# Performance work log

Hardware: AMD Instinct MI355X
Metric: run time of the kernel (lower is better)

## Reference

```python
import jax, jax.numpy as jnp
import numpy as np

H = 16          # num_attention_heads
D = 64          # attention_head_size
BUCKET = 128    # bucket_size
MAX_BUCKETS = 32
TEMP = 0.75
SINKHORN_ITERS = 5
NOISE_KEY = 42  # fixed key for gumbel routing noise (deterministic reference)


def _sinkhorn_route(pl, W, key):
    # pl: [b,h,buckets,d] bucket summaries, W: [h,d,buckets]
    R = jnp.einsum('bhid,hdf->bhif', pl, W)  # [b,h,buckets,buckets]
    u = jax.random.uniform(key, R.shape, R.dtype)
    gumbel = -jnp.log(-jnp.log(u + 1e-6) + 1e-6)
    R = (R + gumbel) / TEMP
    for _ in range(SINKHORN_ITERS):
        R = R - jax.scipy.special.logsumexp(R, axis=-1, keepdims=True)
        R = R - jax.scipy.special.logsumexp(R, axis=-2, keepdims=True)
    return jnp.exp(R)


def setup_inputs() -> dict:
    key = jax.random.key(0)
    kq, kk, kv, kwk, kwv = jax.random.split(key, 5)
    q = jax.random.normal(kq, (64, 4096, 64), jnp.float32)
    k = jax.random.normal(kk, (64, 4096, 64), jnp.float32)
    v = jax.random.normal(kv, (64, 4096, 64), jnp.float32)
    W_keys = jax.random.normal(kwk, (H, D, MAX_BUCKETS), jnp.float32)
    W_vals = jax.random.normal(kwv, (H, D, MAX_BUCKETS), jnp.float32)
    return {'q': q, 'k': k, 'v': v, 'W_keys': W_keys, 'W_vals': W_vals}


def reference(q, q_unused=None, *, _=None, **__):
    raise RuntimeError  # placeholder, replaced below


def reference(q, k, v, W_keys, W_vals):
    t, d = q.shape[1], q.shape[2]
    buckets = t // BUCKET
    # [b, h, buckets, bucket_size, d]
    b_q = q.reshape(-1, H, buckets, BUCKET, d)
    b_k = k.reshape(-1, H, buckets, BUCKET, d)
    b_v = v.reshape(-1, H, buckets, BUCKET, d)

    pl_k = b_k.sum(axis=-2)  # [b,h,buckets,d]
    R_k = _sinkhorn_route(pl_k, W_keys[..., :buckets], jax.random.key(NOISE_KEY))
    # NOTE: original also computes R_v / b_v_r but never uses them for output.

    b_k = jnp.einsum('bhij,bhjsd->bhisd', R_k, b_k) + b_k

    dots = jnp.einsum('bhuid,bhujd->bhuij', b_q, b_k) * (d ** -0.5)
    probs = jax.nn.softmax(dots, axis=-1)
    out = jnp.einsum('bhuij,bhujd->bhuid', probs, b_v)  # [b,h,buckets,s,d]
    return out.reshape(-1, t, d)
```

## Files before the change

### kernel.cpp

```cpp
#include <hip/hip_runtime.h>
#include <math.h>

#define BH 64
#define NB 32
#define BS 128
#define DHEAD 64

typedef __attribute__((ext_vector_type(8))) short bf16x8;
typedef __attribute__((ext_vector_type(4))) float f32x4;

#define LDVT 128
#define LDP 136


__device__ __forceinline__ unsigned rotl32(unsigned x, int d) {
    return (x << d) | (x >> (32 - d));
}

__device__ __forceinline__ void threefry2x32(unsigned k0, unsigned k1,
                                             unsigned& x0, unsigned& x1) {
    const unsigned ks0 = k0, ks1 = k1, ks2 = k0 ^ k1 ^ 0x1BD11BDAu;
    const int r0[4] = {13, 15, 26, 6};
    const int r1[4] = {17, 29, 16, 24};
    x0 += ks0; x1 += ks1;
    #pragma unroll
    for (int i = 0; i < 4; i++) { x0 += x1; x1 = rotl32(x1, r0[i]); x1 ^= x0; }
    x0 += ks1; x1 += ks2 + 1u;
    #pragma unroll
    for (int i = 0; i < 4; i++) { x0 += x1; x1 = rotl32(x1, r1[i]); x1 ^= x0; }
    x0 += ks2; x1 += ks0 + 2u;
    #pragma unroll
    for (int i = 0; i < 4; i++) { x0 += x1; x1 = rotl32(x1, r0[i]); x1 ^= x0; }
    x0 += ks0; x1 += ks1 + 3u;
    #pragma unroll
    for (int i = 0; i < 4; i++) { x0 += x1; x1 = rotl32(x1, r1[i]); x1 ^= x0; }
    x0 += ks1; x1 += ks2 + 4u;
    #pragma unroll
    for (int i = 0; i < 4; i++) { x0 += x1; x1 = rotl32(x1, r0[i]); x1 ^= x0; }
    x0 += ks2; x1 += ks0 + 5u;
}

__device__ __forceinline__ float jax_uniform_part(unsigned f) {
    unsigned x0 = 0u, x1 = f;
    threefry2x32(0u, 42u, x0, x1);
    unsigned bits = x0 ^ x1;
    return __uint_as_float((bits >> 9) | 0x3F800000u) - 1.0f;
}

__global__ void __launch_bounds__(256)
pl_kernel(const float* __restrict__ k, float* __restrict__ pl) {
    int blk = blockIdx.x;
    int g = threadIdx.x >> 6;
    int d = threadIdx.x & 63;
    const float* kp = k + (size_t)blk * 8192 + (size_t)g * 2048 + d;
    float s = 0.f;
    #pragma unroll
    for (int i = 0; i < 32; i++) s += kp[i * 64];
    __shared__ float red[4][64];
    red[g][d] = s;
    __syncthreads();
    if (threadIdx.x < 64)
        pl[blk * 64 + threadIdx.x] = (red[0][threadIdx.x] + red[1][threadIdx.x])
                                   + (red[2][threadIdx.x] + red[3][threadIdx.x]);
}

__global__ void route_kernel(const float* __restrict__ pl, const float* __restrict__ Wk,
                             float* __restrict__ Rout) {
    int bh = blockIdx.x;
    int h = bh & 15;
    int tid = threadIdx.x;
    int i = tid >> 5, j = tid & 31;

    __shared__ float plS[NB * DHEAD];
    __shared__ float T[32 * 33];
    __shared__ float colL[32];

    for (int x = tid; x < NB * DHEAD; x += 1024) plS[x] = pl[bh * NB * DHEAD + x];
    __syncthreads();

    float acc = 0.f;
    #pragma unroll 8
    for (int d2 = 0; d2 < DHEAD; d2++)
        acc += plS[i * DHEAD + d2] * Wk[(h * DHEAD + d2) * NB + j];

    unsigned f = (unsigned)bh * 1024u + (unsigned)i * 32u + (unsigned)j;
    float u = jax_uniform_part(f);
    float g = -logf(-logf(u + 1e-6f) + 1e-6f);
    float val = (acc + g) / 0.75f;

    for (int it = 0; it < 5; it++) {
        float m = val;
        #pragma unroll
        for (int off = 1; off < 32; off <<= 1) m = fmaxf(m, __shfl_xor(m, off, 32));
        float s = expf(val - m);
        #pragma unroll
        for (int off = 1; off < 32; off <<= 1) s += __shfl_xor(s, off, 32);
        val -= m + logf(s);

        T[i * 33 + j] = val;
        __syncthreads();
        float tv = T[j * 33 + i];
        float m2 = tv;
        #pragma unroll
        for (int off = 1; off < 32; off <<= 1) m2 = fmaxf(m2, __shfl_xor(m2, off, 32));
        float s2 = expf(tv - m2);
        #pragma unroll
        for (int off = 1; off < 32; off <<= 1) s2 += __shfl_xor(s2, off, 32);
        if (j == 0) colL[i] = m2 + logf(s2);
        __syncthreads();
        val -= colL[j];
    }
    Rout[bh * 1024 + i * 32 + j] = expf(val) + (i == j ? 1.0f : 0.0f);
}

__global__ void __launch_bounds__(256)
mix_kernel(const float* __restrict__ k, const float* __restrict__ Rp,
           unsigned short* __restrict__ khl) {
    __shared__ float X[32][260];
    int bh = blockIdx.x >> 5;
    int tile = blockIdx.x & 31;
    const size_t kbase = (size_t)bh * 262144;
    const int col0 = tile * 256;

    {
        int j = threadIdx.x >> 3;
        int cs = (threadIdx.x & 7) * 32;
        const float4* src = (const float4*)(k + kbase + (size_t)j * 8192 + col0 + cs);
        #pragma unroll
        for (int t = 0; t < 8; t++)
            *((float4*)&X[j][cs + 4 * t]) = src[t];
    }
    __syncthreads();

    const int col = threadIdx.x;
    float xv[32];
    #pragma unroll
    for (int j = 0; j < 32; j++) xv[j] = X[j][col];

    const float* Rb = Rp + bh * 1024;
    const int slot = col0 + col;
    const int s = slot >> 6, d = slot & 63;
    const int idx = s * 64 + (d ^ ((s & 7) << 3));

    #pragma unroll 4
    for (int i = 0; i < 32; i++) {
        float acc = 0.f;
        #pragma unroll
        for (int j = 0; j < 32; j++) acc = fmaf(Rb[i * 32 + j], xv[j], acc);
        unsigned kb = __float_as_uint(acc);
        unsigned short hi = (unsigned short)(kb >> 16);
        float rem = acc - __uint_as_float(kb & 0xFFFF0000u);
        unsigned short lo = (unsigned short)(__float_as_uint(rem) >> 16);
        unsigned short* bp = khl + ((size_t)(bh * 32 + i) << 14);
        bp[idx] = hi;
        bp[idx + 8192] = lo;
    }
}

__global__ void __launch_bounds__(256)
attn_mfma_kernel(const float* __restrict__ q, const unsigned short* __restrict__ khl,
                 const float* __restrict__ v, float* __restrict__ out) {
    __shared__ __align__(16) unsigned short smem[8192 + 17408];
    unsigned short* VtS = smem;
    unsigned short* KhS = smem + 8192;
    unsigned short* KlS = smem + 16384;
    unsigned short* PbS = smem + 8192;

    const int tid = threadIdx.x;
    const int w = tid >> 6, lane = tid & 63;
    const int quad = lane >> 4, l15 = lane & 15;
    const int row0 = 32 * w;
    const size_t base = (size_t)blockIdx.x * (BS * DHEAD);

    {
        const char* src = (const char*)(khl + ((size_t)blockIdx.x << 14)) + tid * 16;
        char* dst = (char*)KhS + tid * 16;
        #pragma unroll
        for (int c = 0; c < 8; c++)
            __builtin_amdgcn_global_load_lds(
                (const __attribute__((address_space(1))) unsigned int*)(src + c * 4096),
                (__attribute__((address_space(3))) unsigned int*)(dst + c * 4096),
                16, 0, 0);
    }

    {
        int rp = tid >> 2;
        int c0 = (tid & 3) * 16;
        const float* v0 = v + base + (size_t)(2 * rp) * DHEAD + c0;
        const float* v1 = v0 + DHEAD;
        #pragma unroll
        for (int x = 0; x < 4; x++) {
            float4 a = ((const float4*)v0)[x];
            float4 b = ((const float4*)v1)[x];
            float fa[4] = {a.x, a.y, a.z, a.w};
            float fb[4] = {b.x, b.y, b.z, b.w};
            #pragma unroll
            for (int y = 0; y < 4; y++) {
                int c = c0 + 4 * x + y;
                unsigned lo = (__float_as_uint(fa[y]) + 0x8000u) >> 16;
                unsigned hi = (__float_as_uint(fb[y]) + 0x8000u) >> 16;
                unsigned swz = ((unsigned)((c ^ (c >> 4)) & 15)) << 3;
                unsigned idx = (unsigned)c * LDVT + (((unsigned)(2 * rp)) ^ swz);
                *(unsigned*)&VtS[idx] = lo | (hi << 16);
            }
        }
    }

    bf16x8 qh[2][2], ql[2][2];
    #pragma unroll
    for (int ti = 0; ti < 2; ti++) {
        #pragma unroll
        for (int kk = 0; kk < 2; kk++) {
            const float* qp = q + base + (size_t)(row0 + 16 * ti + l15) * DHEAD
                              + kk * 32 + quad * 8;
            float4 a = ((const float4*)qp)[0];
            float4 b = ((const float4*)qp)[1];
            float f[8] = {a.x, a.y, a.z, a.w, b.x, b.y, b.z, b.w};
            #pragma unroll
            for (int j = 0; j < 8; j++) {
                float qs = f[j] * 0.125f;
                unsigned bits = __float_as_uint(qs);
                unsigned short hi = (unsigned short)(bits >> 16);
                float rem = qs - __uint_as_float(bits & 0xFFFF0000u);
                unsigned short lo = (unsigned short)(__float_as_uint(rem) >> 16);
                qh[ti][kk][j] = (short)hi;
                ql[ti][kk][j] = (short)lo;
            }
        }
    }
    __syncthreads();

    f32x4 acc[2][8];
    #pragma unroll
    for (int ti = 0; ti < 2; ti++)
        #pragma unroll
        for (int tc = 0; tc < 8; tc++)
            acc[ti][tc] = (f32x4){0.f, 0.f, 0.f, 0.f};

    #pragma unroll
    for (int tc = 0; tc < 8; tc++) {
        const int jrow = 16 * tc + l15;
        const int swzk = (jrow & 7) << 3;
        const int rbase = jrow * 64;
        bf16x8 bh0 = *(const bf16x8*)&KhS[rbase + ((quad * 8 + 0)  ^ swzk)];
        bf16x8 bh1 = *(const bf16x8*)&KhS[rbase + ((quad * 8 + 32) ^ swzk)];
        bf16x8 bl0 = *(const bf16x8*)&KlS[rbase + ((quad * 8 + 0)  ^ swzk)];
        bf16x8 bl1 = *(const bf16x8*)&KlS[rbase + ((quad * 8 + 32) ^ swzk)];
        __builtin_amdgcn_s_setprio(1);
        #pragma unroll
        for (int ti = 0; ti < 2; ti++) {
            f32x4 c = acc[ti][tc];
            c = __builtin_amdgcn_mfma_f32_16x16x32_bf16(qh[ti][0], bh0, c, 0, 0, 0);
            c = __builtin_amdgcn_mfma_f32_16x16x32_bf16(qh[ti][1], bh1, c, 0, 0, 0);
            c = __builtin_amdgcn_mfma_f32_16x16x32_bf16(ql[ti][0], bh0, c, 0, 0, 0);
            c = __builtin_amdgcn_mfma_f32_16x16x32_bf16(ql[ti][1], bh1, c, 0, 0, 0);
            c = __builtin_amdgcn_mfma_f32_16x16x32_bf16(qh[ti][0], bl0, c, 0, 0, 0);
            c = __builtin_amdgcn_mfma_f32_16x16x32_bf16(qh[ti][1], bl1, c, 0, 0, 0);
            acc[ti][tc] = c;
        }
        __builtin_amdgcn_s_setprio(0);
    }

    float mrow[2][4], lrow[2][4];
    #pragma unroll
    for (int ti = 0; ti < 2; ti++)
        #pragma unroll
        for (int r = 0; r < 4; r++) {
            float m = acc[ti][0][r];
            #pragma unroll
            for (int tc = 1; tc < 8; tc++) m = fmaxf(m, acc[ti][tc][r]);
            #pragma unroll
            for (int off = 1; off < 16; off <<= 1)
                m = fmaxf(m, __shfl_xor(m, off, 64));
            mrow[ti][r] = m;
        }
    #pragma unroll
    for (int ti = 0; ti < 2; ti++)
        #pragma unroll
        for (int r = 0; r < 4; r++) {
            float s = 0.f;
            #pragma unroll
            for (int tc = 0; tc < 8; tc++) {
                float p = __expf(acc[ti][tc][r] - mrow[ti][r]);
                acc[ti][tc][r] = p;
                s += p;
            }
            #pragma unroll
            for (int off = 1; off < 16; off <<= 1)
                s += __shfl_xor(s, off, 64);
            lrow[ti][r] = s;
        }

    __syncthreads();

    #pragma unroll
    for (int ti = 0; ti < 2; ti++)
        #pragma unroll
        for (int tc = 0; tc < 8; tc++)
            #pragma unroll
            for (int r = 0; r < 4; r++) {
                int prow = row0 + 16 * ti + quad * 4 + r;
                unsigned pb = __float_as_uint(acc[ti][tc][r]);
                PbS[prow * LDP + 16 * tc + l15] = (unsigned short)((pb + 0x8000u) >> 16);
            }
    __syncthreads();

    f32x4 oacc[2][4];
    #pragma unroll
    for (int ti = 0; ti < 2; ti++)
        #pragma unroll
        for (int tc = 0; tc < 4; tc++)
            oacc[ti][tc] = (f32x4){0.f, 0.f, 0.f, 0.f};

    #pragma unroll
    for (int kc = 0; kc < 4; kc++) {
        bf16x8 aP[2];
        #pragma unroll
        for (int ti = 0; ti < 2; ti++)
            aP[ti] = *(const bf16x8*)&PbS[(row0 + 16 * ti + l15) * LDP + kc * 32 + quad * 8];
        __builtin_amdgcn_s_setprio(1);
        #pragma unroll
        for (int tc = 0; tc < 4; tc++) {
            unsigned n = (unsigned)(16 * tc + l15);
            unsigned swz = ((n ^ (n >> 4)) & 15u) << 3;
            unsigned idx = n * LDVT + (((unsigned)(kc * 32 + quad * 8)) ^ swz);
            bf16x8 vb = *(const bf16x8*)&VtS[idx];
            #pragma unroll
            for (int ti = 0; ti < 2; ti++)
                oacc[ti][tc] = __builtin_amdgcn_mfma_f32_16x16x32_bf16(aP[ti], vb, oacc[ti][tc], 0, 0, 0);
        }
        __builtin_amdgcn_s_setprio(0);
    }

    float inv[2][4];
    #pragma unroll
    for (int ti = 0; ti < 2; ti++)
        #pragma unroll
        for (int r = 0; r < 4; r++) inv[ti][r] = 1.0f / lrow[ti][r];

    #pragma unroll
    for (int ti = 0; ti < 2; ti++)
        #pragma unroll
        for (int tc = 0; tc < 4; tc++)
            #pragma unroll
            for (int r = 0; r < 4; r++) {
                int orow = row0 + 16 * ti + quad * 4 + r;
                out[base + (size_t)orow * DHEAD + 16 * tc + l15] = oacc[ti][tc][r] * inv[ti][r];
            }
}

extern "C" void kernel_launch(void* const* d_in, const int* in_sizes, int n_in,
                              void* d_out, int out_size, void* d_ws, size_t ws_size,
                              hipStream_t stream) {
    const float* q  = (const float*)d_in[0];
    const float* k  = (const float*)d_in[1];
    const float* v  = (const float*)d_in[2];
    const float* Wk = (const float*)d_in[3];
    float* out = (float*)d_out;

    unsigned short* khl = (unsigned short*)d_ws;
    float* pl = (float*)(khl + (size_t)33554432);
    float* R  = pl + (size_t)131072;

    pl_kernel<<<dim3(BH * NB), dim3(256), 0, stream>>>(k, pl);
    route_kernel<<<dim3(BH), dim3(1024), 0, stream>>>(pl, Wk, R);
    mix_kernel<<<dim3(BH * NB), dim3(256), 0, stream>>>(k, R, khl);
    attn_mfma_kernel<<<dim3(BH * NB), dim3(256), 0, stream>>>(q, khl, v, out);
}
```

Baseline: 289.6 us.

## Vectorize pl reduction, use fast math in routing, pack bf16 stores in mix

The bucket-sum kernel now loads float4 values and reduces across lanes with shuffles before a small shared-memory combine. The Sinkhorn routing kernel switches expf/logf to the fast __expf/__logf intrinsics, which may slightly change numerical accuracy. The mix kernel pairs adjacent lanes through a shuffle so that even lanes write 32-bit words holding two bf16 halves, halving the number of 16-bit global stores at the cost of idle odd lanes on the store.

```diff
diff --git a/kernel.cpp b/kernel.cpp
--- a/kernel.cpp
+++ b/kernel.cpp
@@ -50,18 +50,33 @@
 __global__ void __launch_bounds__(256)
 pl_kernel(const float* __restrict__ k, float* __restrict__ pl) {
     int blk = blockIdx.x;
-    int g = threadIdx.x >> 6;
-    int d = threadIdx.x & 63;
-    const float* kp = k + (size_t)blk * 8192 + (size_t)g * 2048 + d;
-    float s = 0.f;
-    #pragma unroll
-    for (int i = 0; i < 32; i++) s += kp[i * 64];
-    __shared__ float red[4][64];
-    red[g][d] = s;
-    __syncthreads();
-    if (threadIdx.x < 64)
-        pl[blk * 64 + threadIdx.x] = (red[0][threadIdx.x] + red[1][threadIdx.x])
-                                   + (red[2][threadIdx.x] + red[3][threadIdx.x]);
+    int tid = threadIdx.x;
+    int w = tid >> 6, l = tid & 63;
+    int rcls = l >> 4, c4 = l & 15;
+    const float4* base = (const float4*)(k + (size_t)blk * 8192);
+
+    float4 acc = {0.f, 0.f, 0.f, 0.f};
+    #pragma unroll
+    for (int t = 0; t < 8; t++) {
+        float4 x = base[(w * 32 + t * 4 + rcls) * 16 + c4];
+        acc.x += x.x; acc.y += x.y; acc.z += x.z; acc.w += x.w;
+    }
+    #pragma unroll
+    for (int off = 16; off < 64; off <<= 1) {
+        acc.x += __shfl_xor(acc.x, off);
+        acc.y += __shfl_xor(acc.y, off);
+        acc.z += __shfl_xor(acc.z, off);
+        acc.w += __shfl_xor(acc.w, off);
+    }
+    __shared__ float4 red[4][16];
+    if (rcls == 0) red[w][c4] = acc;
+    __syncthreads();
+    if (tid < 64) {
+        int g = tid >> 2, j = tid & 3;
+        float s = ((const float*)&red[0][g])[j] + ((const float*)&red[1][g])[j]
+                + ((const float*)&red[2][g])[j] + ((const float*)&red[3][g])[j];
+        pl[blk * 64 + tid] = s;
+    }
 }
 
 __global__ void route_kernel(const float* __restrict__ pl, const float* __restrict__ Wk,
@@ -85,17 +100,17 @@
 
     unsigned f = (unsigned)bh * 1024u + (unsigned)i * 32u + (unsigned)j;
     float u = jax_uniform_part(f);
-    float g = -logf(-logf(u + 1e-6f) + 1e-6f);
+    float g = -__logf(-__logf(u + 1e-6f) + 1e-6f);
     float val = (acc + g) / 0.75f;
 
     for (int it = 0; it < 5; it++) {
         float m = val;
         #pragma unroll
         for (int off = 1; off < 32; off <<= 1) m = fmaxf(m, __shfl_xor(m, off, 32));
-        float s = expf(val - m);
+        float s = __expf(val - m);
         #pragma unroll
         for (int off = 1; off < 32; off <<= 1) s += __shfl_xor(s, off, 32);
-        val -= m + logf(s);
+        val -= m + __logf(s);
 
         T[i * 33 + j] = val;
         __syncthreads();
@@ -103,14 +118,14 @@
         float m2 = tv;
         #pragma unroll
         for (int off = 1; off < 32; off <<= 1) m2 = fmaxf(m2, __shfl_xor(m2, off, 32));
-        float s2 = expf(tv - m2);
+        float s2 = __expf(tv - m2);
         #pragma unroll
         for (int off = 1; off < 32; off <<= 1) s2 += __shfl_xor(s2, off, 32);
-        if (j == 0) colL[i] = m2 + logf(s2);
+        if (j == 0) colL[i] = m2 + __logf(s2);
         __syncthreads();
         val -= colL[j];
     }
-    Rout[bh * 1024 + i * 32 + j] = expf(val) + (i == j ? 1.0f : 0.0f);
+    Rout[bh * 1024 + i * 32 + j] = __expf(val) + (i == j ? 1.0f : 0.0f);
 }
 
 __global__ void __launch_bounds__(256)
@@ -141,6 +156,7 @@
     const int slot = col0 + col;
     const int s = slot >> 6, d = slot & 63;
     const int idx = s * 64 + (d ^ ((s & 7) << 3));
+    const bool even = (col & 1) == 0;
 
     #pragma unroll 4
     for (int i = 0; i < 32; i++) {
@@ -148,12 +164,16 @@
         #pragma unroll
         for (int j = 0; j < 32; j++) acc = fmaf(Rb[i * 32 + j], xv[j], acc);
         unsigned kb = __float_as_uint(acc);
-        unsigned short hi = (unsigned short)(kb >> 16);
+        unsigned hiu = kb >> 16;
         float rem = acc - __uint_as_float(kb & 0xFFFF0000u);
-        unsigned short lo = (unsigned short)(__float_as_uint(rem) >> 16);
-        unsigned short* bp = khl + ((size_t)(bh * 32 + i) << 14);
-        bp[idx] = hi;
-        bp[idx + 8192] = lo;
+        unsigned lou = __float_as_uint(rem) >> 16;
+        unsigned oh = (unsigned)__shfl_xor((int)hiu, 1);
+        unsigned ol = (unsigned)__shfl_xor((int)lou, 1);
+        if (even) {
+            unsigned short* bp = khl + ((size_t)(bh * 32 + i) << 14);
+            *(unsigned*)&bp[idx]        = hiu | (oh << 16);
+            *(unsigned*)&bp[idx + 8192] = lou | (ol << 16);
+        }
     }
 }
 
```

Result: faster. 276.3 us (-4.6%).
